# Optimization experiments

Hardware: AMD Instinct MI355X
Metric: run time of the kernel (lower is better)

Reference implementation:

```python
import jax, jax.numpy as jnp
import numpy as np

C = 5.0          # tanh clamp constant (args.c, non-trainable)
B, N, R, D = 4, 16, 64, 256  # batch, block_num, block_len, word_dim
NEG = -1e9


def setup_inputs() -> dict:
    key = jax.random.key(0)
    ks = iter(jax.random.split(key, 80))

    def W(i, o):
        # xavier-like init (torch stores (out,in); we store (in,out) and use x @ W)
        return jax.random.normal(next(ks), (i, o), jnp.float32) * np.float32(np.sqrt(2.0 / (i + o)))

    def bvec(d):
        return jax.random.normal(next(ks), (d,), jnp.float32) * 0.01

    inp = {"x": jax.random.normal(next(ks), (B, N, R, D), jnp.float32)}
    for p in ("fw", "bw"):
        inp[f"fcW_{p}"] = W(D, D);  inp[f"fcb_{p}"] = bvec(D)
        inp[f"mW1_{p}"] = W(D, D);  inp[f"mW2_{p}"] = W(D, D);  inp[f"mb_{p}"] = bvec(D)
        inp[f"s2tW1_{p}"] = W(D, D); inp[f"s2tb1_{p}"] = bvec(D)
        inp[f"s2tW_{p}"] = W(D, D);  inp[f"s2tb_{p}"] = bvec(D)
        inp[f"gW1_{p}"] = W(D, D);  inp[f"gW2_{p}"] = W(D, D);  inp[f"gb_{p}"] = bvec(D)
        inp[f"fW1_{p}"] = W(3 * D, D); inp[f"fb1_{p}"] = bvec(D)
        inp[f"fW2_{p}"] = W(3 * D, D); inp[f"fb2_{p}"] = bvec(D)
    return inp


def _mSA(x, W1, W2, b, fw):
    # x: (..., L, d) -> (..., L, d). Additive per-feature attention with strict
    # triangular mask. fw: token i attends to j > i (last row zeroed);
    # bw: token i attends to j < i (first row zeroed). Matches the torch
    # -inf mask + narrow + zero-pad construction exactly.
    L = x.shape[-2]
    xi = (x @ W1)[..., :, None, :]                 # (..., L, 1, d)
    xj = (x @ W2)[..., None, :, :]                 # (..., 1, L, d)
    f = C * jnp.tanh((xi + xj + b) / C)            # (..., i, j, d)
    i = jnp.arange(L)[:, None]
    j = jnp.arange(L)[None, :]
    allowed = (j > i) if fw else (j < i)           # (L, L)
    scores = jnp.where(allowed[..., None], f, NEG)
    att = jax.nn.softmax(scores, axis=-2)          # softmax over j
    rowvalid = (jnp.arange(L) < L - 1) if fw else (jnp.arange(L) > 0)
    att = att * rowvalid[:, None, None].astype(x.dtype)
    return jnp.einsum('...ijd,...jd->...id', att, x)


def _s2t(x, W1, b1, Wo, bo):
    # source2token self-attention: (..., L, d) -> (..., d)
    f = jax.nn.relu(x @ W1 + b1)
    a = jax.nn.softmax(f @ Wo + bo, axis=-2)
    return jnp.sum(a * x, axis=-2)


def _mblosa(x, mW1, mW2, mb, s2tW1, s2tb1, s2tW, s2tb,
            gW1, gW2, gb, fW1, fb1, fW2, fb2, fw):
    Bb, n, r, d = x.shape
    h = _mSA(x, mW1, mW2, mb, fw)                  # (B, n, r, d) intra-block
    v = _s2t(h, s2tW1, s2tb1, s2tW, s2tb)          # (B, n, d)    block summary
    o = _mSA(v, mW1, mW2, mb, fw)                  # (B, n, d)    inter-block
    G = jax.nn.sigmoid(o @ gW1 + v @ gW2 + gb)
    e = G * o + (1.0 - G) * v                      # (B, n, d)
    # torch: cat of e[i] repeated r times, then narrow(1, 0, n)
    idx = jnp.arange(n) // r
    E = e[:, idx]                                  # (B, n, d)
    # torch: flatten blocks then narrow(1, 0, n) (faithful to source)
    xf = x.reshape(Bb, n * r, d)[:, :n]
    hf = h.reshape(Bb, n * r, d)[:, :n]
    cat = jnp.concatenate([xf, hf, E], axis=-1)    # (B, n, 3d)
    fusion = jax.nn.relu(cat @ fW1 + fb1)
    Gf = jax.nn.sigmoid(cat @ fW2 + fb2)
    return Gf * fusion + (1.0 - Gf) * xf           # (B, n, d)


def reference(x,
              fcW_fw, fcb_fw, mW1_fw, mW2_fw, mb_fw, s2tW1_fw, s2tb1_fw,
              s2tW_fw, s2tb_fw, gW1_fw, gW2_fw, gb_fw, fW1_fw, fb1_fw,
              fW2_fw, fb2_fw,
              fcW_bw, fcb_bw, mW1_bw, mW2_bw, mb_bw, s2tW1_bw, s2tb1_bw,
              s2tW_bw, s2tb_bw, gW1_bw, gW2_bw, gb_bw, fW1_bw, fb1_bw,
              fW2_bw, fb2_bw):
    in_fw = jax.nn.relu(x @ fcW_fw + fcb_fw)
    in_bw = jax.nn.relu(x @ fcW_bw + fcb_bw)
    u_fw = _mblosa(in_fw, mW1_fw, mW2_fw, mb_fw, s2tW1_fw, s2tb1_fw,
                   s2tW_fw, s2tb_fw, gW1_fw, gW2_fw, gb_fw,
                   fW1_fw, fb1_fw, fW2_fw, fb2_fw, True)
    u_bw = _mblosa(in_bw, mW1_bw, mW2_bw, mb_bw, s2tW1_bw, s2tb1_bw,
                   s2tW_bw, s2tb_bw, gW1_bw, gW2_bw, gb_bw,
                   fW1_bw, fb1_bw, fW2_bw, fb2_bw, False)
    return jnp.concatenate([u_fw, u_bw], axis=-1)  # (B, n, 2d)
```

## Files before the change

### kernel.cpp

```cpp
#include <hip/hip_runtime.h>
#include <hip/hip_bf16.h>

typedef __hip_bfloat16 BF16;
typedef __attribute__((ext_vector_type(8))) short short8;
typedef __attribute__((ext_vector_type(4))) float f32x4;

#define MFMA_B16(a,b,c) __builtin_amdgcn_mfma_f32_16x16x32_bf16((a),(b),(c),0,0,0)

__device__ __forceinline__ short f2bs(float f){ BF16 h = __float2bfloat16(f); return *(short*)&h; }
__device__ __forceinline__ float bs2f(short s){ BF16 h = *(BF16*)&s; return __bfloat162float(h); }

struct SrcPack { const float* s[10]; };

__global__ __launch_bounds__(256) void transpose_k(SrcPack p, short* __restrict__ Oh,
                                                   short* __restrict__ Ol)
{
    __shared__ float s[64][65];
    const float* W = p.s[blockIdx.y];
    short* oh = Oh + (size_t)blockIdx.y * 65536;
    short* ol = Ol + (size_t)blockIdx.y * 65536;
    int tr = (blockIdx.x >> 2) * 64, tc = (blockIdx.x & 3) * 64;
    #pragma unroll
    for (int i = 0; i < 16; i++) {
        int e = threadIdx.x + i * 256;
        int r = e >> 6, c = e & 63;
        s[c][r] = W[(size_t)(tr + r) * 256 + tc + c];
    }
    __syncthreads();
    #pragma unroll
    for (int i = 0; i < 16; i++) {
        int e = threadIdx.x + i * 256;
        int c2 = e >> 6, r2 = e & 63;
        float v = s[c2][r2];
        short hi = f2bs(v);
        short lo = f2bs(v - bs2f(hi));
        size_t oi = (size_t)(tc + c2) * 256 + tr + r2;
        oh[oi] = hi;
        ol[oi] = lo;
    }
}

template<int AM, int OM, int RELU>
__device__ __forceinline__ void gemm_body(const void* __restrict__ A0,
    const void* __restrict__ Alo,
    const short* __restrict__ Wh, const short* __restrict__ Wl,
    const float* __restrict__ bias, void* __restrict__ O0, void* __restrict__ O1,
    int row0, int col0)
{
    constexpr int LDK = 72;
    __shared__ short sAh[64 * LDK];
    __shared__ short sAl[(AM == 0) ? 8 : 64 * LDK];
    __shared__ short sBh[64 * LDK];
    __shared__ short sBl[64 * LDK];
    int tid = threadIdx.x;
    int w = tid >> 6, l = tid & 63;
    int m = l & 15, q = l >> 4;
    int sr = w * 16 + m;

    f32x4 acc[4];
    #pragma unroll
    for (int cf = 0; cf < 4; cf++) acc[cf] = (f32x4)(0.f);

    for (int kh = 0; kh < 4; kh++) {
        int kbase = kh * 64;
        #pragma unroll
        for (int i = 0; i < 2; i++) {
            int kl = q * 8 + 32 * i;
            size_t gofs = (size_t)(row0 + sr) * 256 + kbase + kl;
            if (AM == 1) {
                const float* src = (const float*)A0 + gofs;
                float4 f0 = *(const float4*)src;
                float4 f1 = *(const float4*)(src + 4);
                short8 vh, vl;
                float tmp[8] = {f0.x, f0.y, f0.z, f0.w, f1.x, f1.y, f1.z, f1.w};
                #pragma unroll
                for (int j = 0; j < 8; j++) {
                    vh[j] = f2bs(tmp[j]);
                    vl[j] = f2bs(tmp[j] - bs2f(vh[j]));
                }
                *(short8*)&sAh[sr * LDK + kl] = vh;
                *(short8*)&sAl[sr * LDK + kl] = vl;
            } else if (AM == 2) {
                *(short8*)&sAh[sr * LDK + kl] = *(const short8*)((const short*)A0 + gofs);
                *(short8*)&sAl[sr * LDK + kl] = *(const short8*)((const short*)Alo + gofs);
            } else {
                *(short8*)&sAh[sr * LDK + kl] = *(const short8*)((const short*)A0 + gofs);
            }
            size_t gofsB = (size_t)(col0 + sr) * 256 + kbase + kl;
            *(short8*)&sBh[sr * LDK + kl] = *(const short8*)(Wh + gofsB);
            *(short8*)&sBl[sr * LDK + kl] = *(const short8*)(Wl + gofsB);
        }
        __syncthreads();
        #pragma unroll
        for (int ch = 0; ch < 2; ch++) {
            int k = ch * 32 + q * 8;
            short8 ah = *(const short8*)&sAh[(w * 16 + m) * LDK + k];
            short8 al = (AM != 0) ? *(const short8*)&sAl[(w * 16 + m) * LDK + k] : ah;
            #pragma unroll
            for (int cf = 0; cf < 4; cf++) {
                short8 bh = *(const short8*)&sBh[(cf * 16 + m) * LDK + k];
                short8 bl = *(const short8*)&sBl[(cf * 16 + m) * LDK + k];
                acc[cf] = MFMA_B16(ah, bh, acc[cf]);
                acc[cf] = MFMA_B16(ah, bl, acc[cf]);
                if (AM != 0)
                    acc[cf] = MFMA_B16(al, bh, acc[cf]);
            }
        }
        __syncthreads();
    }
    #pragma unroll
    for (int cf = 0; cf < 4; cf++) {
        int col = col0 + cf * 16 + m;
        float bv = bias ? bias[col] : 0.f;
        #pragma unroll
        for (int r = 0; r < 4; r++) {
            int row = row0 + w * 16 + q * 4 + r;
            float v = acc[cf][r] + bv;
            if (RELU) v = fmaxf(v, 0.f);
            size_t oi = (size_t)row * 256 + col;
            if (OM == 0) {
                ((float*)O0)[oi] = v;
            } else if (OM == 1) {
                ((short*)O0)[oi] = f2bs(v);
            } else {
                short hi = f2bs(v);
                ((short*)O0)[oi] = hi;
                ((short*)O1)[oi] = f2bs(v - bs2f(hi));
            }
        }
    }
}

struct GDir { const void* A0; const void* Al; const short* Wh; const short* Wl;
              const float* bias; void* O0; void* O1; };

template<int AM, int OM, int RELU>
__global__ __launch_bounds__(256) void gemm_k(GDir p0, GDir p1)
{
    GDir p = blockIdx.z ? p1 : p0;
    gemm_body<AM, OM, RELU>(p.A0, p.Al, p.Wh, p.Wl, p.bias, p.O0, p.O1,
                            blockIdx.x * 64, blockIdx.y * 64);
}

struct G2Dir { const float* A; const short* W1h; const short* W1l;
               const short* W2h; const short* W2l; const float* b2;
               float* C1; float* C2; };

__global__ __launch_bounds__(256) void gemm2s_k(G2Dir p0, G2Dir p1)
{
    G2Dir p = blockIdx.z ? p1 : p0;
    int y = blockIdx.y;
    const short* Wh = (y < 4) ? p.W1h : p.W2h;
    const short* Wl = (y < 4) ? p.W1l : p.W2l;
    void* C = (y < 4) ? (void*)p.C1 : (void*)p.C2;
    const float* bias = (y < 4) ? nullptr : p.b2;
    gemm_body<1, 0, 0>(p.A, nullptr, Wh, Wl, bias, C, nullptr, 0, (y & 3) * 64);
}

struct MbloDir { const short* Ah; const short* Al;
                 const short* W1h; const short* W1l;
                 const short* W2h; const short* W2l;
                 const float* mb; short* Hh; short* Hl; int fw; };

__global__ __launch_bounds__(256) void mblo_k(MbloDir p0, MbloDir p1)
{
    __shared__ char smraw[55296] __attribute__((aligned(16)));
    short* gAh  = (short*)smraw;
    short* gAl  = gAh + 4608;
    short* gB1h = gAh + 9216;
    short* gB1l = gAh + 13824;
    short* gB2h = gAh + 18432;
    short* gB2l = gAh + 23040;
    float* aP = (float*)smraw;
    float* aQ = aP + 4352;
    float* aX = aP + 8704;

    MbloDir p = blockIdx.z ? p1 : p0;
    int tid = threadIdx.x;
    int w = tid >> 6, l = tid & 63;
    int m = l & 15, q = l >> 4;
    int sr = w * 16 + m;
    int row0 = blockIdx.x * 64, d0 = blockIdx.y * 64;

    f32x4 acc1[4], acc2[4];
    #pragma unroll
    for (int cf = 0; cf < 4; cf++) { acc1[cf] = (f32x4)(0.f); acc2[cf] = (f32x4)(0.f); }

    for (int kh = 0; kh < 4; kh++) {
        int kbase = kh * 64;
        #pragma unroll
        for (int i = 0; i < 2; i++) {
            int kl = q * 8 + 32 * i;
            size_t ga = (size_t)(row0 + sr) * 256 + kbase + kl;
            *(short8*)&gAh[sr * 72 + kl] = *(const short8*)(p.Ah + ga);
            *(short8*)&gAl[sr * 72 + kl] = *(const short8*)(p.Al + ga);
            size_t gb = (size_t)(d0 + sr) * 256 + kbase + kl;
            *(short8*)&gB1h[sr * 72 + kl] = *(const short8*)(p.W1h + gb);
            *(short8*)&gB1l[sr * 72 + kl] = *(const short8*)(p.W1l + gb);
            *(short8*)&gB2h[sr * 72 + kl] = *(const short8*)(p.W2h + gb);
            *(short8*)&gB2l[sr * 72 + kl] = *(const short8*)(p.W2l + gb);
        }
        __syncthreads();
        #pragma unroll
        for (int ch = 0; ch < 2; ch++) {
            int k = ch * 32 + q * 8;
            short8 ah = *(const short8*)&gAh[(w * 16 + m) * 72 + k];
            short8 al = *(const short8*)&gAl[(w * 16 + m) * 72 + k];
            #pragma unroll
            for (int cf = 0; cf < 4; cf++) {
                int bofs = (cf * 16 + m) * 72 + k;
                short8 b1h = *(const short8*)&gB1h[bofs];
                short8 b1l = *(const short8*)&gB1l[bofs];
                acc1[cf] = MFMA_B16(ah, b1h, acc1[cf]);
                acc1[cf] = MFMA_B16(ah, b1l, acc1[cf]);
                acc1[cf] = MFMA_B16(al, b1h, acc1[cf]);
                short8 b2h = *(const short8*)&gB2h[bofs];
                short8 b2l = *(const short8*)&gB2l[bofs];
                acc2[cf] = MFMA_B16(ah, b2h, acc2[cf]);
                acc2[cf] = MFMA_B16(ah, b2l, acc2[cf]);
                acc2[cf] = MFMA_B16(al, b2h, acc2[cf]);
            }
        }
        __syncthreads();
    }
    #pragma unroll
    for (int cf = 0; cf < 4; cf++) {
        int col = cf * 16 + m;
        float mbv = p.mb[d0 + col];
        #pragma unroll
        for (int r = 0; r < 4; r++) {
            int row = w * 16 + q * 4 + r;
            aP[row * 68 + col] = __expf(0.4f * acc1[cf][r]);
            aQ[row * 68 + col] = __expf(0.4f * (acc2[cf][r] + mbv));
        }
    }
    #pragma unroll
    for (int it = 0; it < 2; it++) {
        int e = tid + it * 256;
        int j = e >> 3, d8 = (e & 7) * 8;
        short8 xh = *(const short8*)(p.Ah + (size_t)(row0 + j) * 256 + d0 + d8);
        short8 xl = *(const short8*)(p.Al + (size_t)(row0 + j) * 256 + d0 + d8);
        #pragma unroll
        for (int t = 0; t < 8; t++)
            aX[j * 68 + d8 + t] = bs2f(xh[t]) + bs2f(xl[t]);
    }
    __syncthreads();
    for (int t = 0; t < 16; t++) {
        int i = w + 4 * t;
        float P = aP[i * 68 + l];
        int js = p.fw ? (i + 1) : 0;
        int je = p.fw ? 64 : i;
        float den = 0.f, num = 0.f;
        for (int j = js; j < je; j++) {
            float u = P * aQ[j * 68 + l];
            float r = __builtin_amdgcn_rcpf(1.f + u);
            float wgt = __expf(-10.f * r);
            den += wgt;
            num += wgt * aX[j * 68 + l];
        }
        float out = (je > js) ? (num * __builtin_amdgcn_rcpf(den)) : 0.f;
        short hi = f2bs(out);
        size_t oi = (size_t)(row0 + i) * 256 + d0 + l;
        p.Hh[oi] = hi;
        p.Hl[oi] = f2bs(out - bs2f(hi));
    }
}

struct PoolDir { const short* T1; const short* Wh; const short* Wl; const float* bias;
                 const short* Hh; const short* Hl; float* V; };

__global__ __launch_bounds__(256) void s2t_pool_k(PoolDir p0, PoolDir p1)
{
    __shared__ char smraw[37888] __attribute__((aligned(16)));
    short* gAh = (short*)smraw;
    short* gBh = gAh + 4608;
    short* gBl = gAh + 9216;
    float* aL = (float*)smraw;
    float* aH = aL + 4352;
    float* rm = aL + 8704;
    float* rd = aL + 8960;
    float* rn = aL + 9216;

    PoolDir p = blockIdx.z ? p1 : p0;
    int tid = threadIdx.x;
    int w = tid >> 6, l = tid & 63;
    int m = l & 15, q = l >> 4;
    int sr = w * 16 + m;
    int row0 = blockIdx.x * 64, d0 = blockIdx.y * 64;

    f32x4 acc[4];
    #pragma unroll
    for (int cf = 0; cf < 4; cf++) acc[cf] = (f32x4)(0.f);

    for (int kh = 0; kh < 4; kh++) {
        int kbase = kh * 64;
        #pragma unroll
        for (int i = 0; i < 2; i++) {
            int kl = q * 8 + 32 * i;
            *(short8*)&gAh[sr * 72 + kl] =
                *(const short8*)(p.T1 + (size_t)(row0 + sr) * 256 + kbase + kl);
            size_t gb = (size_t)(d0 + sr) * 256 + kbase + kl;
            *(short8*)&gBh[sr * 72 + kl] = *(const short8*)(p.Wh + gb);
            *(short8*)&gBl[sr * 72 + kl] = *(const short8*)(p.Wl + gb);
        }
        __syncthreads();
        #pragma unroll
        for (int ch = 0; ch < 2; ch++) {
            int k = ch * 32 + q * 8;
            short8 ah = *(const short8*)&gAh[(w * 16 + m) * 72 + k];
            #pragma unroll
            for (int cf = 0; cf < 4; cf++) {
                int bofs = (cf * 16 + m) * 72 + k;
                short8 bh = *(const short8*)&gBh[bofs];
                short8 bl = *(const short8*)&gBl[bofs];
                acc[cf] = MFMA_B16(ah, bh, acc[cf]);
                acc[cf] = MFMA_B16(ah, bl, acc[cf]);
            }
        }
        __syncthreads();
    }
    #pragma unroll
    for (int cf = 0; cf < 4; cf++) {
        int col = cf * 16 + m;
        float bv = p.bias[d0 + col];
        #pragma unroll
        for (int r = 0; r < 4; r++) {
            int row = w * 16 + q * 4 + r;
            aL[row * 68 + col] = acc[cf][r] + bv;
        }
    }
    #pragma unroll
    for (int it = 0; it < 2; it++) {
        int e = tid + it * 256;
        int j = e >> 3, d8 = (e & 7) * 8;
        short8 xh = *(const short8*)(p.Hh + (size_t)(row0 + j) * 256 + d0 + d8);
        short8 xl = *(const short8*)(p.Hl + (size_t)(row0 + j) * 256 + d0 + d8);
        #pragma unroll
        for (int t = 0; t < 8; t++)
            aH[j * 68 + d8 + t] = bs2f(xh[t]) + bs2f(xl[t]);
    }
    __syncthreads();
    int dl = tid & 63, rq = tid >> 6;
    float mx = -1e30f, den = 0.f, num = 0.f;
    #pragma unroll
    for (int rr = 0; rr < 16; rr++) {
        int r = rq * 16 + rr;
        float lv = aL[r * 68 + dl];
        float hv = aH[r * 68 + dl];
        if (lv > mx) {
            float sc = __expf(mx - lv);
            den *= sc; num *= sc; mx = lv;
        }
        float wgt = __expf(lv - mx);
        den += wgt; num += wgt * hv;
    }
    rm[rq * 64 + dl] = mx; rd[rq * 64 + dl] = den; rn[rq * 64 + dl] = num;
    __syncthreads();
    if (rq == 0) {
        float M = fmaxf(fmaxf(rm[dl], rm[64 + dl]), fmaxf(rm[128 + dl], rm[192 + dl]));
        float D = 0.f, Nn = 0.f;
        #pragma unroll
        for (int k = 0; k < 4; k++) {
            float sc = __expf(rm[k * 64 + dl] - M);
            D += rd[k * 64 + dl] * sc;
            Nn += rn[k * 64 + dl] * sc;
        }
        p.V[(size_t)blockIdx.x * 256 + d0 + dl] = Nn / D;
    }
}

struct GateDir { const float* vW1; const float* vW2; const float* V;
                 const float* gW1; const float* gW2; const float* gb;
                 float* E0; int fw; };

__global__ __launch_bounds__(256) void attn2gate_k(GateDir p0, GateDir p1)
{
    GateDir p = blockIdx.z ? p1 : p0;
    __shared__ float so[256], sv[256], red[4][64];
    int b = blockIdx.x, k = threadIdx.x;
    float o = 0.f;
    if (p.fw) {
        float qv = p.vW1[(size_t)(b * 16) * 256 + k];
        float den = 0.f, num = 0.f;
        for (int j = 1; j < 16; j++) {
            float z = (qv + p.vW2[(size_t)(b * 16 + j) * 256 + k]) * 0.2f;
            float e2 = __expf(2.f * z);
            float t = 1.f - 2.f / (e2 + 1.f);
            float wgt = __expf(5.f * t);
            den += wgt; num += wgt * p.V[(size_t)(b * 16 + j) * 256 + k];
        }
        o = num / den;
    }
    so[k] = o;
    sv[k] = p.V[(size_t)(b * 16) * 256 + k];
    __syncthreads();
    int c = k & 63, ks = k >> 6;
    int gc = blockIdx.y * 64 + c;
    float acc = 0.f;
    int k0 = ks * 64;
    #pragma unroll 8
    for (int kk = 0; kk < 64; kk++) {
        int kx = k0 + kk;
        acc += so[kx] * p.gW1[(size_t)kx * 256 + gc] + sv[kx] * p.gW2[(size_t)kx * 256 + gc];
    }
    red[ks][c] = acc;
    __syncthreads();
    if (ks == 0) {
        float a = red[0][c] + red[1][c] + red[2][c] + red[3][c] + p.gb[gc];
        float G = 1.f / (1.f + __expf(-a));
        p.E0[b * 256 + gc] = G * so[gc] + (1.f - G) * sv[gc];
    }
}

struct FuseDir { const short* INh; const short* INl; const short* Hh; const short* Hl;
                 const float* E0; const float* fW1; const float* fb1;
                 const float* fW2; const float* fb2; };

__global__ __launch_bounds__(256) void fusion_k(FuseDir p0, FuseDir p1, float* __restrict__ out)
{
    FuseDir p = blockIdx.z ? p1 : p0;
    __shared__ float cat[768];
    __shared__ float red1[4][64], red2[4][64];
    int bt = blockIdx.x, b = bt >> 4, t = bt & 15;
    int c = threadIdx.x & 63, ks = threadIdx.x >> 6;
    int gc = blockIdx.y * 64 + c;
    size_t xrow = ((size_t)b * 1024 + t) * 256;
    cat[threadIdx.x]       = bs2f(p.INh[xrow + threadIdx.x]) + bs2f(p.INl[xrow + threadIdx.x]);
    cat[256 + threadIdx.x] = bs2f(p.Hh[xrow + threadIdx.x]) + bs2f(p.Hl[xrow + threadIdx.x]);
    cat[512 + threadIdx.x] = p.E0[b * 256 + threadIdx.x];
    __syncthreads();
    float a1 = 0.f, a2 = 0.f;
    int k0 = ks * 192;
    #pragma unroll 8
    for (int kk = 0; kk < 192; kk++) {
        int k = k0 + kk;
        float cv = cat[k];
        a1 += cv * p.fW1[(size_t)k * 256 + gc];
        a2 += cv * p.fW2[(size_t)k * 256 + gc];
    }
    red1[ks][c] = a1; red2[ks][c] = a2;
    __syncthreads();
    if (ks == 0) {
        float s1 = red1[0][c] + red1[1][c] + red1[2][c] + red1[3][c] + p.fb1[gc];
        float s2 = red2[0][c] + red2[1][c] + red2[2][c] + red2[3][c] + p.fb2[gc];
        float fus = fmaxf(s1, 0.f);
        float Gf = 1.f / (1.f + __expf(-s2));
        float u = Gf * fus + (1.f - Gf) * cat[gc];
        out[((size_t)(b * 16 + t)) * 512 + (size_t)blockIdx.z * 256 + gc] = u;
    }
}

extern "C" void kernel_launch(void* const* d_in, const int* in_sizes, int n_in,
                              void* d_out, int out_size, void* d_ws, size_t ws_size,
                              hipStream_t stream)
{
    const float* x = (const float*)d_in[0];
    char* base = (char*)d_ws;
    auto alloc = [&](size_t bytes){ void* r = base; base += (bytes + 255) & ~255ULL; return r; };
    short* inH = (short*)alloc(2 * 1048576 * 2);
    short* inL = (short*)alloc(2 * 1048576 * 2);
    short* hH  = (short*)alloc(2 * 1048576 * 2);
    short* hL  = (short*)alloc(2 * 1048576 * 2);
    short* t1  = (short*)alloc(2 * 1048576 * 2);
    short* wtH = (short*)alloc(10 * 65536 * 2);
    short* wtL = (short*)alloc(10 * 65536 * 2);
    float* v   = (float*)alloc(2 * 16384 * 4);
    float* vW1 = (float*)alloc(2 * 16384 * 4);
    float* vW2 = (float*)alloc(2 * 16384 * 4);
    float* E0  = (float*)alloc(2 * 1024 * 4);

    SrcPack sp;
    const int src_idx[5] = {0, 2, 3, 5, 7};
    for (int p = 0; p < 2; p++)
        for (int i = 0; i < 5; i++)
            sp.s[p * 5 + i] = (const float*)d_in[1 + p * 16 + src_idx[i]];
    transpose_k<<<dim3(16, 10), 256, 0, stream>>>(sp, wtH, wtL);

    GDir fc[2], s2t1[2];
    MbloDir mbd[2];
    PoolDir pld[2];
    G2Dir g2d[2];
    GateDir gtd[2];
    FuseDir fsd[2];
    for (int p = 0; p < 2; p++) {
        int bi = 1 + p * 16;
        const float* fcb   = (const float*)d_in[bi + 1];
        const float* mb    = (const float*)d_in[bi + 4];
        const float* s2tb1 = (const float*)d_in[bi + 6];
        const float* s2tb  = (const float*)d_in[bi + 8];
        size_t po = (size_t)p * 1048576;
        const short* W0h = wtH + (size_t)(p * 5 + 0) * 65536, *W0l = wtL + (size_t)(p * 5 + 0) * 65536;
        const short* W1h = wtH + (size_t)(p * 5 + 1) * 65536, *W1l = wtL + (size_t)(p * 5 + 1) * 65536;
        const short* W2h = wtH + (size_t)(p * 5 + 2) * 65536, *W2l = wtL + (size_t)(p * 5 + 2) * 65536;
        const short* W3h = wtH + (size_t)(p * 5 + 3) * 65536, *W3l = wtL + (size_t)(p * 5 + 3) * 65536;
        const short* W4h = wtH + (size_t)(p * 5 + 4) * 65536, *W4l = wtL + (size_t)(p * 5 + 4) * 65536;

        fc[p]   = { x, nullptr, W0h, W0l, fcb, inH + po, inL + po };
        mbd[p]  = { inH + po, inL + po, W1h, W1l, W2h, W2l, mb, hH + po, hL + po, (p == 0) };
        s2t1[p] = { hH + po, hL + po, W3h, W3l, s2tb1, t1 + po, nullptr };
        pld[p]  = { t1 + po, W4h, W4l, s2tb, hH + po, hL + po, v + p * 16384 };
        g2d[p]  = { v + p * 16384, W1h, W1l, W2h, W2l, mb, vW1 + p * 16384, vW2 + p * 16384 };
        gtd[p]  = { vW1 + p * 16384, vW2 + p * 16384, v + p * 16384,
                    (const float*)d_in[bi + 9], (const float*)d_in[bi + 10],
                    (const float*)d_in[bi + 11], E0 + p * 1024, (p == 0) };
        fsd[p]  = { inH + po, inL + po, hH + po, hL + po, E0 + p * 1024,
                    (const float*)d_in[bi + 12], (const float*)d_in[bi + 13],
                    (const float*)d_in[bi + 14], (const float*)d_in[bi + 15] };
    }

    gemm_k<1, 2, 1><<<dim3(64, 4, 2), 256, 0, stream>>>(fc[0], fc[1]);
    mblo_k<<<dim3(64, 4, 2), 256, 0, stream>>>(mbd[0], mbd[1]);
    gemm_k<2, 1, 1><<<dim3(64, 4, 2), 256, 0, stream>>>(s2t1[0], s2t1[1]);
    s2t_pool_k<<<dim3(64, 4, 2), 256, 0, stream>>>(pld[0], pld[1]);
    gemm2s_k<<<dim3(1, 8, 2), 256, 0, stream>>>(g2d[0], g2d[1]);
    attn2gate_k<<<dim3(4, 4, 2), 256, 0, stream>>>(gtd[0], gtd[1]);
    fusion_k<<<dim3(64, 4, 2), 256, 0, stream>>>(fsd[0], fsd[1], (float*)d_out);
}
```

Before: 225.8 us.

## Drop low-part weight MFMAs in mSA and s2t GEMMs, widen mSA block to 512

The mSA projection GEMMs and the first s2t GEMM now use only the bf16 high part of the weights, so the ah*bl MFMA term and its shared-memory tile are dropped. The activation low part is still kept. mblo_k moves to 512 threads: each wave covers a 16x32 output sub-tile, staging loads are simplified, the attention loop uses 8 rows per wave, and the shared-memory row pad goes from 68 to 64. This cuts MFMA work and weight traffic and raises parallelism in the attention reduction, at the cost of weight-precision accuracy and possible bank conflicts from the unpadded stride.

```diff
diff --git a/kernel.cpp b/kernel.cpp
--- a/kernel.cpp
+++ b/kernel.cpp
@@ -40,7 +40,7 @@
     }
 }
 
-template<int AM, int OM, int RELU>
+template<int AM, int OM, int RELU, int BS>
 __device__ __forceinline__ void gemm_body(const void* __restrict__ A0,
     const void* __restrict__ Alo,
     const short* __restrict__ Wh, const short* __restrict__ Wl,
@@ -51,7 +51,7 @@
     __shared__ short sAh[64 * LDK];
     __shared__ short sAl[(AM == 0) ? 8 : 64 * LDK];
     __shared__ short sBh[64 * LDK];
-    __shared__ short sBl[64 * LDK];
+    __shared__ short sBl[BS ? 8 : 64 * LDK];
     int tid = threadIdx.x;
     int w = tid >> 6, l = tid & 63;
     int m = l & 15, q = l >> 4;
@@ -88,7 +88,8 @@
             }
             size_t gofsB = (size_t)(col0 + sr) * 256 + kbase + kl;
             *(short8*)&sBh[sr * LDK + kl] = *(const short8*)(Wh + gofsB);
-            *(short8*)&sBl[sr * LDK + kl] = *(const short8*)(Wl + gofsB);
+            if (!BS)
+                *(short8*)&sBl[sr * LDK + kl] = *(const short8*)(Wl + gofsB);
         }
         __syncthreads();
         #pragma unroll
@@ -99,9 +100,11 @@
             #pragma unroll
             for (int cf = 0; cf < 4; cf++) {
                 short8 bh = *(const short8*)&sBh[(cf * 16 + m) * LDK + k];
-                short8 bl = *(const short8*)&sBl[(cf * 16 + m) * LDK + k];
                 acc[cf] = MFMA_B16(ah, bh, acc[cf]);
-                acc[cf] = MFMA_B16(ah, bl, acc[cf]);
+                if (!BS) {
+                    short8 bl = *(const short8*)&sBl[(cf * 16 + m) * LDK + k];
+                    acc[cf] = MFMA_B16(ah, bl, acc[cf]);
+                }
                 if (AM != 0)
                     acc[cf] = MFMA_B16(al, bh, acc[cf]);
             }
@@ -134,12 +137,12 @@
 struct GDir { const void* A0; const void* Al; const short* Wh; const short* Wl;
               const float* bias; void* O0; void* O1; };
 
-template<int AM, int OM, int RELU>
+template<int AM, int OM, int RELU, int BS>
 __global__ __launch_bounds__(256) void gemm_k(GDir p0, GDir p1)
 {
     GDir p = blockIdx.z ? p1 : p0;
-    gemm_body<AM, OM, RELU>(p.A0, p.Al, p.Wh, p.Wl, p.bias, p.O0, p.O1,
-                            blockIdx.x * 64, blockIdx.y * 64);
+    gemm_body<AM, OM, RELU, BS>(p.A0, p.Al, p.Wh, p.Wl, p.bias, p.O0, p.O1,
+                                blockIdx.x * 64, blockIdx.y * 64);
 }
 
 struct G2Dir { const float* A; const short* W1h; const short* W1l;
@@ -154,109 +157,98 @@
     const short* Wl = (y < 4) ? p.W1l : p.W2l;
     void* C = (y < 4) ? (void*)p.C1 : (void*)p.C2;
     const float* bias = (y < 4) ? nullptr : p.b2;
-    gemm_body<1, 0, 0>(p.A, nullptr, Wh, Wl, bias, C, nullptr, 0, (y & 3) * 64);
+    gemm_body<1, 0, 0, 0>(p.A, nullptr, Wh, Wl, bias, C, nullptr, 0, (y & 3) * 64);
 }
 
 struct MbloDir { const short* Ah; const short* Al;
-                 const short* W1h; const short* W1l;
-                 const short* W2h; const short* W2l;
+                 const short* W1h; const short* W2h;
                  const float* mb; short* Hh; short* Hl; int fw; };
 
-__global__ __launch_bounds__(256) void mblo_k(MbloDir p0, MbloDir p1)
-{
-    __shared__ char smraw[55296] __attribute__((aligned(16)));
+__global__ __launch_bounds__(512) void mblo_k(MbloDir p0, MbloDir p1)
+{
+    __shared__ char smraw[49152] __attribute__((aligned(16)));
     short* gAh  = (short*)smraw;
     short* gAl  = gAh + 4608;
     short* gB1h = gAh + 9216;
-    short* gB1l = gAh + 13824;
-    short* gB2h = gAh + 18432;
-    short* gB2l = gAh + 23040;
+    short* gB2h = gAh + 13824;
     float* aP = (float*)smraw;
-    float* aQ = aP + 4352;
-    float* aX = aP + 8704;
+    float* aQ = aP + 4096;
+    float* aX = aP + 8192;
 
     MbloDir p = blockIdx.z ? p1 : p0;
     int tid = threadIdx.x;
     int w = tid >> 6, l = tid & 63;
     int m = l & 15, q = l >> 4;
-    int sr = w * 16 + m;
+    int rh = w >> 1;
+    int cb = (w & 1) * 2;
     int row0 = blockIdx.x * 64, d0 = blockIdx.y * 64;
-
-    f32x4 acc1[4], acc2[4];
-    #pragma unroll
-    for (int cf = 0; cf < 4; cf++) { acc1[cf] = (f32x4)(0.f); acc2[cf] = (f32x4)(0.f); }
+    int srow = tid >> 3;
+    int skl  = (tid & 7) * 8;
+
+    f32x4 acc1[2], acc2[2];
+    #pragma unroll
+    for (int cf = 0; cf < 2; cf++) { acc1[cf] = (f32x4)(0.f); acc2[cf] = (f32x4)(0.f); }
 
     for (int kh = 0; kh < 4; kh++) {
         int kbase = kh * 64;
-        #pragma unroll
-        for (int i = 0; i < 2; i++) {
-            int kl = q * 8 + 32 * i;
-            size_t ga = (size_t)(row0 + sr) * 256 + kbase + kl;
-            *(short8*)&gAh[sr * 72 + kl] = *(const short8*)(p.Ah + ga);
-            *(short8*)&gAl[sr * 72 + kl] = *(const short8*)(p.Al + ga);
-            size_t gb = (size_t)(d0 + sr) * 256 + kbase + kl;
-            *(short8*)&gB1h[sr * 72 + kl] = *(const short8*)(p.W1h + gb);
-            *(short8*)&gB1l[sr * 72 + kl] = *(const short8*)(p.W1l + gb);
-            *(short8*)&gB2h[sr * 72 + kl] = *(const short8*)(p.W2h + gb);
-            *(short8*)&gB2l[sr * 72 + kl] = *(const short8*)(p.W2l + gb);
-        }
+        size_t ga = (size_t)(row0 + srow) * 256 + kbase + skl;
+        *(short8*)&gAh[srow * 72 + skl] = *(const short8*)(p.Ah + ga);
+        *(short8*)&gAl[srow * 72 + skl] = *(const short8*)(p.Al + ga);
+        size_t gb = (size_t)(d0 + srow) * 256 + kbase + skl;
+        *(short8*)&gB1h[srow * 72 + skl] = *(const short8*)(p.W1h + gb);
+        *(short8*)&gB2h[srow * 72 + skl] = *(const short8*)(p.W2h + gb);
         __syncthreads();
         #pragma unroll
         for (int ch = 0; ch < 2; ch++) {
             int k = ch * 32 + q * 8;
-            short8 ah = *(const short8*)&gAh[(w * 16 + m) * 72 + k];
-            short8 al = *(const short8*)&gAl[(w * 16 + m) * 72 + k];
+            short8 ah = *(const short8*)&gAh[(rh * 16 + m) * 72 + k];
+            short8 al = *(const short8*)&gAl[(rh * 16 + m) * 72 + k];
             #pragma unroll
-            for (int cf = 0; cf < 4; cf++) {
-                int bofs = (cf * 16 + m) * 72 + k;
-                short8 b1h = *(const short8*)&gB1h[bofs];
-                short8 b1l = *(const short8*)&gB1l[bofs];
-                acc1[cf] = MFMA_B16(ah, b1h, acc1[cf]);
-                acc1[cf] = MFMA_B16(ah, b1l, acc1[cf]);
-                acc1[cf] = MFMA_B16(al, b1h, acc1[cf]);
-                short8 b2h = *(const short8*)&gB2h[bofs];
-                short8 b2l = *(const short8*)&gB2l[bofs];
-                acc2[cf] = MFMA_B16(ah, b2h, acc2[cf]);
-                acc2[cf] = MFMA_B16(ah, b2l, acc2[cf]);
-                acc2[cf] = MFMA_B16(al, b2h, acc2[cf]);
+            for (int cf = 0; cf < 2; cf++) {
+                int bofs = ((cb + cf) * 16 + m) * 72 + k;
+                short8 b1 = *(const short8*)&gB1h[bofs];
+                acc1[cf] = MFMA_B16(ah, b1, acc1[cf]);
+                acc1[cf] = MFMA_B16(al, b1, acc1[cf]);
+                short8 b2 = *(const short8*)&gB2h[bofs];
+                acc2[cf] = MFMA_B16(ah, b2, acc2[cf]);
+                acc2[cf] = MFMA_B16(al, b2, acc2[cf]);
             }
         }
         __syncthreads();
     }
     #pragma unroll
-    for (int cf = 0; cf < 4; cf++) {
-        int col = cf * 16 + m;
+    for (int cf = 0; cf < 2; cf++) {
+        int col = (cb + cf) * 16 + m;
         float mbv = p.mb[d0 + col];
         #pragma unroll
         for (int r = 0; r < 4; r++) {
-            int row = w * 16 + q * 4 + r;
-            aP[row * 68 + col] = __expf(0.4f * acc1[cf][r]);
-            aQ[row * 68 + col] = __expf(0.4f * (acc2[cf][r] + mbv));
-        }
-    }
-    #pragma unroll
-    for (int it = 0; it < 2; it++) {
-        int e = tid + it * 256;
-        int j = e >> 3, d8 = (e & 7) * 8;
-        short8 xh = *(const short8*)(p.Ah + (size_t)(row0 + j) * 256 + d0 + d8);
-        short8 xl = *(const short8*)(p.Al + (size_t)(row0 + j) * 256 + d0 + d8);
+            int row = rh * 16 + q * 4 + r;
+            aP[row * 64 + col] = __expf(0.4f * acc1[cf][r]);
+            aQ[row * 64 + col] = __expf(0.4f * (acc2[cf][r] + mbv));
+        }
+    }
+    {
+        size_t gx = (size_t)(row0 + srow) * 256 + d0 + skl;
+        short8 xh = *(const short8*)(p.Ah + gx);
+        short8 xl = *(const short8*)(p.Al + gx);
         #pragma unroll
         for (int t = 0; t < 8; t++)
-            aX[j * 68 + d8 + t] = bs2f(xh[t]) + bs2f(xl[t]);
-    }
-    __syncthreads();
-    for (int t = 0; t < 16; t++) {
-        int i = w + 4 * t;
-        float P = aP[i * 68 + l];
+            aX[srow * 64 + skl + t] = bs2f(xh[t]) + bs2f(xl[t]);
+    }
+    __syncthreads();
+    #pragma unroll
+    for (int t = 0; t < 8; t++) {
+        int i = w + 8 * t;
+        float P = aP[i * 64 + l];
         int js = p.fw ? (i + 1) : 0;
         int je = p.fw ? 64 : i;
         float den = 0.f, num = 0.f;
         for (int j = js; j < je; j++) {
-            float u = P * aQ[j * 68 + l];
+            float u = P * aQ[j * 64 + l];
             float r = __builtin_amdgcn_rcpf(1.f + u);
             float wgt = __expf(-10.f * r);
             den += wgt;
-            num += wgt * aX[j * 68 + l];
+            num += wgt * aX[j * 64 + l];
         }
         float out = (je > js) ? (num * __builtin_amdgcn_rcpf(den)) : 0.f;
         short hi = f2bs(out);
@@ -492,12 +484,12 @@
         const short* W0h = wtH + (size_t)(p * 5 + 0) * 65536, *W0l = wtL + (size_t)(p * 5 + 0) * 65536;
         const short* W1h = wtH + (size_t)(p * 5 + 1) * 65536, *W1l = wtL + (size_t)(p * 5 + 1) * 65536;
         const short* W2h = wtH + (size_t)(p * 5 + 2) * 65536, *W2l = wtL + (size_t)(p * 5 + 2) * 65536;
-        const short* W3h = wtH + (size_t)(p * 5 + 3) * 65536, *W3l = wtL + (size_t)(p * 5 + 3) * 65536;
+        const short* W3h = wtH + (size_t)(p * 5 + 3) * 65536;
         const short* W4h = wtH + (size_t)(p * 5 + 4) * 65536, *W4l = wtL + (size_t)(p * 5 + 4) * 65536;
 
         fc[p]   = { x, nullptr, W0h, W0l, fcb, inH + po, inL + po };
-        mbd[p]  = { inH + po, inL + po, W1h, W1l, W2h, W2l, mb, hH + po, hL + po, (p == 0) };
-        s2t1[p] = { hH + po, hL + po, W3h, W3l, s2tb1, t1 + po, nullptr };
+        mbd[p]  = { inH + po, inL + po, W1h, W2h, mb, hH + po, hL + po, (p == 0) };
+        s2t1[p] = { hH + po, hL + po, W3h, nullptr, s2tb1, t1 + po, nullptr };
         pld[p]  = { t1 + po, W4h, W4l, s2tb, hH + po, hL + po, v + p * 16384 };
         g2d[p]  = { v + p * 16384, W1h, W1l, W2h, W2l, mb, vW1 + p * 16384, vW2 + p * 16384 };
         gtd[p]  = { vW1 + p * 16384, vW2 + p * 16384, v + p * 16384,
@@ -508,9 +500,9 @@
                     (const float*)d_in[bi + 14], (const float*)d_in[bi + 15] };
     }
 
-    gemm_k<1, 2, 1><<<dim3(64, 4, 2), 256, 0, stream>>>(fc[0], fc[1]);
-    mblo_k<<<dim3(64, 4, 2), 256, 0, stream>>>(mbd[0], mbd[1]);
-    gemm_k<2, 1, 1><<<dim3(64, 4, 2), 256, 0, stream>>>(s2t1[0], s2t1[1]);
+    gemm_k<1, 2, 1, 0><<<dim3(64, 4, 2), 256, 0, stream>>>(fc[0], fc[1]);
+    mblo_k<<<dim3(64, 4, 2), 512, 0, stream>>>(mbd[0], mbd[1]);
+    gemm_k<2, 1, 1, 1><<<dim3(64, 4, 2), 256, 0, stream>>>(s2t1[0], s2t1[1]);
     s2t_pool_k<<<dim3(64, 4, 2), 256, 0, stream>>>(pld[0], pld[1]);
     gemm2s_k<<<dim3(1, 8, 2), 256, 0, stream>>>(g2d[0], g2d[1]);
     attn2gate_k<<<dim3(4, 4, 2), 256, 0, stream>>>(gtd[0], gtd[1]);
```

Result: faster. 211.9 us (-6.1%).
